# Kernel optimization log

Hardware: AMD Instinct MI355X
Metric: run time of the kernel (lower is better)

## Reference

```python
import jax, jax.numpy as jnp
import numpy as np

B, T_STEPS, H, W = 8192, 512, 64, 64


def setup_inputs() -> dict:
    key = jax.random.key(0)
    k_w, k_g, k_i, k_j, k_a = jax.random.split(key, 5)
    walls = (jax.random.uniform(k_w, (B, H, W)) < 0.3).astype(jnp.float32)
    walls = walls.at[:, 0, :].set(1.0).at[:, H - 1, :].set(1.0)
    walls = walls.at[:, :, 0].set(1.0).at[:, :, W - 1].set(1.0)
    # goals: sparse cells with value 10 (the code checks goals[...] == 10)
    goals = jnp.where(jax.random.uniform(k_g, (B, H, W)) < 0.02, 10.0, 0.0).astype(jnp.float32)
    # start positions strictly interior; clear the wall at each start cell
    i0 = jax.random.randint(k_i, (B,), 1, H - 1)
    j0 = jax.random.randint(k_j, (B,), 1, W - 1)
    walls = walls.at[jnp.arange(B), i0, j0].set(0.0)
    world = jnp.stack([walls, goals], axis=1)  # [B, 2, H, W]
    s0 = jnp.stack([i0, j0], axis=1).astype(jnp.float32)  # [B, 2]
    a = jax.random.randint(k_a, (B, T_STEPS), 0, 5).astype(jnp.int32)  # actions in {0..4}
    return {"s0": s0, "a": a, "world": world, "T": T_STEPS}


def _rollout(s0, a, world, T):
    walls = world[:, 0].reshape(world.shape[0], -1)  # [B, H*W]
    goals = world[:, 1].reshape(world.shape[0], -1)  # [B, H*W]
    Wd = world.shape[3]

    def step(s, a_t):
        # action deltas: 1 -> row-1, 2 -> row+1, 3 -> col-1, 4 -> col+1, 0 -> stay
        dr = jnp.where(a_t == 1, -1.0, jnp.where(a_t == 2, 1.0, 0.0))
        dc = jnp.where(a_t == 3, -1.0, jnp.where(a_t == 4, 1.0, 0.0))
        s_new = s + jnp.stack([dr, dc], axis=1).astype(s.dtype)  # [B, 2]
        idx = (s_new[:, 0].astype(jnp.int32) * Wd + s_new[:, 1].astype(jnp.int32))[:, None]
        g = jnp.take_along_axis(goals, idx, axis=1)[:, 0]
        w = jnp.take_along_axis(walls, idx, axis=1)[:, 0]
        hit_goal = g == 10.0
        hit_wall = jnp.logical_and(jnp.logical_not(hit_goal), w == 1.0)
        r = jnp.where(hit_goal, 1.0, jnp.where(hit_wall, -1.0, -0.01)).astype(jnp.float32)
        s_next = jnp.where(hit_wall[:, None], s, s_new)  # revert move on wall hit
        return s_next, (s_next, r)

    _, (s_traj, r_traj) = jax.lax.scan(step, s0, jnp.swapaxes(a[:, :T], 0, 1))
    s_full = jnp.concatenate([s0[:, None, :], jnp.swapaxes(s_traj, 0, 1)], axis=1)  # [B, T+1, 2]
    r0 = jnp.zeros((s0.shape[0], 1), dtype=jnp.float32)
    r_full = jnp.concatenate([r0, jnp.swapaxes(r_traj, 0, 1)], axis=1)  # [B, T+1]
    return s_full, r_full


def reference(s0, a, world, T):
    return _rollout(s0, a, world, T)
```

## Files before the change

kernel.cpp:

```cpp
#include <hip/hip_runtime.h>
#include <stdint.h>

#define T_STEPS 512
#define CELLS   4096
#define EPB     32
#define WPE     256
#define WPAD    257
#define ASTRIDE 130
#define SSTRIDE 66
#define RSTRIDE 33
#define CHUNK   32
#define NCHUNK  (T_STEPS / CHUNK)
#define KPC     (CHUNK / 4)

__device__ __forceinline__ uint32_t code4(float4 w, float4 g) {
    uint32_t b0 = (g.x == 10.0f) ? 2u : ((w.x == 1.0f) ? 1u : 0u);
    uint32_t b1 = (g.y == 10.0f) ? 2u : ((w.y == 1.0f) ? 1u : 0u);
    uint32_t b2 = (g.z == 10.0f) ? 2u : ((w.z == 1.0f) ? 1u : 0u);
    uint32_t b3 = (g.w == 10.0f) ? 2u : ((w.w == 1.0f) ? 1u : 0u);
    return b0 | (b1 << 2) | (b2 << 4) | (b3 << 6);
}

__global__ __launch_bounds__(64) void pack_kernel(
    const float* __restrict__ world, uint32_t* __restrict__ packed)
{
    const int b = blockIdx.x;
    const int t = threadIdx.x;
    const float* wbase = world + (size_t)b * (2 * CELLS);
    const float* gbase = wbase + CELLS;
    #pragma unroll
    for (int h = 0; h < 4; ++h) {
        const int w  = h * 64 + t;
        const int c0 = w * 16;
        uint32_t word = 0;
        #pragma unroll
        for (int j = 0; j < 4; ++j) {
            float4 wf = *(const float4*)(wbase + c0 + 4 * j);
            float4 gf = *(const float4*)(gbase + c0 + 4 * j);
            word |= code4(wf, gf) << (8 * j);
        }
        packed[(size_t)b * WPE + w] = word;
    }
}

__global__ __launch_bounds__(64) void rollout_kernel(
    const float* __restrict__ s0,
    const int*   __restrict__ act,
    const uint32_t* __restrict__ packed,
    float* __restrict__ out,
    int B)
{
    __shared__ uint32_t wlds[EPB * WPAD];
    __shared__ uint32_t alds[EPB * ASTRIDE];
    __shared__ float    sbuf[EPB * SSTRIDE];
    __shared__ float    rbuf[EPB * RSTRIDE];

    const int tid = threadIdx.x;
    const int b0  = blockIdx.x * EPB;

    for (int ee = 0; ee < EPB; ++ee) {
        uint4 v = *(const uint4*)(packed + (size_t)(b0 + ee) * WPE + tid * 4);
        const int base = ee * WPAD + tid * 4;
        wlds[base]     = v.x;
        wlds[base + 1] = v.y;
        wlds[base + 2] = v.z;
        wlds[base + 3] = v.w;
    }
    for (int ee = 0; ee < EPB; ++ee) {
        const int4* ap = (const int4*)(act + (size_t)(b0 + ee) * T_STEPS);
        const int4 x = ap[2 * tid];
        const int4 y = ap[2 * tid + 1];
        const uint32_t w0 = (uint32_t)(x.x & 255) | ((uint32_t)(x.y & 255) << 8)
                          | ((uint32_t)(x.z & 255) << 16) | ((uint32_t)(x.w & 255) << 24);
        const uint32_t w1 = (uint32_t)(y.x & 255) | ((uint32_t)(y.y & 255) << 8)
                          | ((uint32_t)(y.z & 255) << 16) | ((uint32_t)(y.w & 255) << 24);
        const int base = ee * ASTRIDE + 2 * tid;
        alds[base]     = w0;
        alds[base + 1] = w1;
    }
    __syncthreads();

    const int e = tid & (EPB - 1);
    const int b = b0 + e;
    float2 s = *(const float2*)(s0 + 2 * (size_t)b);
    int r = (int)s.x;
    int c = (int)s.y;
    int p = r * 64 + c;
    const uint32_t* my    = wlds + e * WPAD;
    const uint32_t* myact = alds + e * ASTRIDE;

    auto lookup = [&](int q) -> int {
        const int idx = q + ((q < 0) ? CELLS : 0);
        const uint32_t wd = my[(idx >> 4) & (WPE - 1)];
        const int cell = (wd >> ((idx & 15) * 2)) & 3;
        return ((unsigned)idx < (unsigned)CELLS) ? cell : 0;
    };

    float* const s_base = out;
    float* const r_base = out + (size_t)B * (2 * (T_STEPS + 1));

    if (tid < EPB) {
        *(float2*)(s_base + (size_t)b * (2 * (T_STEPS + 1))) = s;
        r_base[(size_t)b * (T_STEPS + 1)] = 0.0f;
    }

    uint32_t aw = myact[0];
    for (int chunk = 0; chunk < NCHUNK; ++chunk) {
        for (int k = 0; k < KPC; ++k) {
            const int kk = chunk * KPC + k;
            const uint32_t aw_next = myact[kk + 1];
            const int a0 = aw & 255, a1 = (aw >> 8) & 255;
            const int a2 = (aw >> 16) & 255, a3 = (aw >> 24) & 255;
            const int as4[4] = {a0, a1, a2, a3};
            #pragma unroll
            for (int jj = 0; jj < 2; ++jj) {
                const int ls = k * 4 + jj * 2;
                const int u0 = as4[2 * jj];
                const int u1 = as4[2 * jj + 1];
                const int d0r = (u0 == 1) ? -1 : ((u0 == 2) ? 1 : 0);
                const int d0c = (u0 == 3) ? -1 : ((u0 == 4) ? 1 : 0);
                const int d1r = (u1 == 1) ? -1 : ((u1 == 2) ? 1 : 0);
                const int d1c = (u1 == 3) ? -1 : ((u1 == 4) ? 1 : 0);
                const int e0 = d0r * 64 + d0c;
                const int e1 = d1r * 64 + d1c;
                const int q0  = p + e0;
                const int q10 = p + e1;
                const int q11 = q0 + e1;
                const int l0  = lookup(q0);
                const int l10 = lookup(q10);
                const int l11 = lookup(q11);
                const bool hw0  = (l0 == 1);
                const float rew0 = (l0 == 2) ? 1.0f : (hw0 ? -1.0f : -0.01f);
                const int p0  = hw0 ? p : q0;
                const int r0v = hw0 ? r : r + d0r;
                const int c0v = hw0 ? c : c + d0c;
                const int l1 = hw0 ? l10 : l11;
                const bool hw1  = (l1 == 1);
                const float rew1 = (l1 == 2) ? 1.0f : (hw1 ? -1.0f : -0.01f);
                p = hw1 ? p0 : p0 + e1;
                r = hw1 ? r0v : r0v + d1r;
                c = hw1 ? c0v : c0v + d1c;
                *(float2*)(&sbuf[e * SSTRIDE + 2 * ls]) =
                    make_float2((float)r0v, (float)c0v);
                *(float2*)(&sbuf[e * SSTRIDE + 2 * ls + 2]) =
                    make_float2((float)r, (float)c);
                rbuf[e * RSTRIDE + ls]     = rew0;
                rbuf[e * RSTRIDE + ls + 1] = rew1;
            }
            aw = aw_next;
        }
        __syncthreads();
        for (int ee = 0; ee < EPB; ++ee) {
            const float v = sbuf[ee * SSTRIDE + tid];
            s_base[(size_t)(b0 + ee) * (2 * (T_STEPS + 1)) + chunk * 64 + 2 + tid] = v;
        }
        for (int ee = 0; ee < EPB; ee += 2) {
            const int e2 = ee + (tid >> 5);
            const int j  = tid & 31;
            const float v = rbuf[e2 * RSTRIDE + j];
            r_base[(size_t)(b0 + e2) * (T_STEPS + 1) + chunk * 32 + 1 + j] = v;
        }
        __syncthreads();
    }
}

extern "C" void kernel_launch(void* const* d_in, const int* in_sizes, int n_in,
                              void* d_out, int out_size, void* d_ws, size_t ws_size,
                              hipStream_t stream) {
    const float* s0    = (const float*)d_in[0];
    const int*   act   = (const int*)d_in[1];
    const float* world = (const float*)d_in[2];
    float*       out   = (float*)d_out;
    uint32_t*    packed = (uint32_t*)d_ws;

    const int B = in_sizes[0] / 2;

    pack_kernel<<<B, 64, 0, stream>>>(world, packed);
    rollout_kernel<<<B / EPB, 64, 0, stream>>>(s0, act, packed, out, B);
}
```

Measured before the change: 443.8 us.

## Interleave two environments per lane and use a zero sentinel word for out-of-range lookups

Previously lanes 32-63 duplicated the work of lanes 0-31. Now each of the 16 lane groups steps two environments at once, interleaving their independent LDS lookups to raise ILP across the serial dependency chain. Out-of-range indices now read a padded sentinel word set to zero, replacing the per-lookup clamp-and-select. Each lane does twice as many serial steps, and lanes 16-63 all repeat the same work, so overall throughput depends on latency hiding.

New measurement: 475.6 us. +7.2%, slower.

```diff
diff --git a/kernel.cpp b/kernel.cpp
--- a/kernel.cpp
+++ b/kernel.cpp
@@ -66,6 +66,7 @@
         wlds[base + 2] = v.z;
         wlds[base + 3] = v.w;
     }
+    if (tid < EPB) wlds[tid * WPAD + WPE] = 0u;
     for (int ee = 0; ee < EPB; ++ee) {
         const int4* ap = (const int4*)(act + (size_t)(b0 + ee) * T_STEPS);
         const int4 x = ap[2 * tid];
@@ -80,74 +81,112 @@
     }
     __syncthreads();
 
-    const int e = tid & (EPB - 1);
-    const int b = b0 + e;
-    float2 s = *(const float2*)(s0 + 2 * (size_t)b);
-    int r = (int)s.x;
-    int c = (int)s.y;
-    int p = r * 64 + c;
-    const uint32_t* my    = wlds + e * WPAD;
-    const uint32_t* myact = alds + e * ASTRIDE;
-
-    auto lookup = [&](int q) -> int {
-        const int idx = q + ((q < 0) ? CELLS : 0);
-        const uint32_t wd = my[(idx >> 4) & (WPE - 1)];
-        const int cell = (wd >> ((idx & 15) * 2)) & 3;
-        return ((unsigned)idx < (unsigned)CELLS) ? cell : 0;
-    };
-
     float* const s_base = out;
     float* const r_base = out + (size_t)B * (2 * (T_STEPS + 1));
 
     if (tid < EPB) {
-        *(float2*)(s_base + (size_t)b * (2 * (T_STEPS + 1))) = s;
-        r_base[(size_t)b * (T_STEPS + 1)] = 0.0f;
-    }
-
-    uint32_t aw = myact[0];
+        const float2 si = *(const float2*)(s0 + 2 * (size_t)(b0 + tid));
+        *(float2*)(s_base + (size_t)(b0 + tid) * (2 * (T_STEPS + 1))) = si;
+        r_base[(size_t)(b0 + tid) * (T_STEPS + 1)] = 0.0f;
+    }
+
+    const int eA = 2 * (tid & 15);
+    const int eB = eA + 1;
+    const float2 sA = *(const float2*)(s0 + 2 * (size_t)(b0 + eA));
+    const float2 sB = *(const float2*)(s0 + 2 * (size_t)(b0 + eB));
+    int rA = (int)sA.x, cA = (int)sA.y, pA = rA * 64 + cA;
+    int rB = (int)sB.x, cB = (int)sB.y, pB = rB * 64 + cB;
+    const uint32_t* myA = wlds + eA * WPAD;
+    const uint32_t* myB = wlds + eB * WPAD;
+    const uint32_t* actA = alds + eA * ASTRIDE;
+    const uint32_t* actB = alds + eB * ASTRIDE;
+
+    auto waddr = [](int q) -> int {
+        const int w = (int)((((unsigned)q) >> 4) & 255u);
+        return ((unsigned)(q + CELLS) < 2u * CELLS) ? w : WPE;
+    };
+
+    uint32_t awA = actA[0];
+    uint32_t awB = actB[0];
     for (int chunk = 0; chunk < NCHUNK; ++chunk) {
         for (int k = 0; k < KPC; ++k) {
             const int kk = chunk * KPC + k;
-            const uint32_t aw_next = myact[kk + 1];
-            const int a0 = aw & 255, a1 = (aw >> 8) & 255;
-            const int a2 = (aw >> 16) & 255, a3 = (aw >> 24) & 255;
-            const int as4[4] = {a0, a1, a2, a3};
+            const uint32_t awA_n = actA[kk + 1];
+            const uint32_t awB_n = actB[kk + 1];
+            const int aA[4] = {(int)(awA & 255), (int)((awA >> 8) & 255),
+                               (int)((awA >> 16) & 255), (int)((awA >> 24) & 255)};
+            const int aB[4] = {(int)(awB & 255), (int)((awB >> 8) & 255),
+                               (int)((awB >> 16) & 255), (int)((awB >> 24) & 255)};
             #pragma unroll
             for (int jj = 0; jj < 2; ++jj) {
                 const int ls = k * 4 + jj * 2;
-                const int u0 = as4[2 * jj];
-                const int u1 = as4[2 * jj + 1];
-                const int d0r = (u0 == 1) ? -1 : ((u0 == 2) ? 1 : 0);
-                const int d0c = (u0 == 3) ? -1 : ((u0 == 4) ? 1 : 0);
-                const int d1r = (u1 == 1) ? -1 : ((u1 == 2) ? 1 : 0);
-                const int d1c = (u1 == 3) ? -1 : ((u1 == 4) ? 1 : 0);
-                const int e0 = d0r * 64 + d0c;
-                const int e1 = d1r * 64 + d1c;
-                const int q0  = p + e0;
-                const int q10 = p + e1;
-                const int q11 = q0 + e1;
-                const int l0  = lookup(q0);
-                const int l10 = lookup(q10);
-                const int l11 = lookup(q11);
-                const bool hw0  = (l0 == 1);
-                const float rew0 = (l0 == 2) ? 1.0f : (hw0 ? -1.0f : -0.01f);
-                const int p0  = hw0 ? p : q0;
-                const int r0v = hw0 ? r : r + d0r;
-                const int c0v = hw0 ? c : c + d0c;
-                const int l1 = hw0 ? l10 : l11;
-                const bool hw1  = (l1 == 1);
-                const float rew1 = (l1 == 2) ? 1.0f : (hw1 ? -1.0f : -0.01f);
-                p = hw1 ? p0 : p0 + e1;
-                r = hw1 ? r0v : r0v + d1r;
-                c = hw1 ? c0v : c0v + d1c;
-                *(float2*)(&sbuf[e * SSTRIDE + 2 * ls]) =
-                    make_float2((float)r0v, (float)c0v);
-                *(float2*)(&sbuf[e * SSTRIDE + 2 * ls + 2]) =
-                    make_float2((float)r, (float)c);
-                rbuf[e * RSTRIDE + ls]     = rew0;
-                rbuf[e * RSTRIDE + ls + 1] = rew1;
+                const int uA0 = aA[2 * jj], uA1 = aA[2 * jj + 1];
+                const int uB0 = aB[2 * jj], uB1 = aB[2 * jj + 1];
+                const int dA0r = (uA0 == 1) ? -1 : ((uA0 == 2) ? 1 : 0);
+                const int dA0c = (uA0 == 3) ? -1 : ((uA0 == 4) ? 1 : 0);
+                const int dA1r = (uA1 == 1) ? -1 : ((uA1 == 2) ? 1 : 0);
+                const int dA1c = (uA1 == 3) ? -1 : ((uA1 == 4) ? 1 : 0);
+                const int dB0r = (uB0 == 1) ? -1 : ((uB0 == 2) ? 1 : 0);
+                const int dB0c = (uB0 == 3) ? -1 : ((uB0 == 4) ? 1 : 0);
+                const int dB1r = (uB1 == 1) ? -1 : ((uB1 == 2) ? 1 : 0);
+                const int dB1c = (uB1 == 3) ? -1 : ((uB1 == 4) ? 1 : 0);
+                const int eAd0 = dA0r * 64 + dA0c, eAd1 = dA1r * 64 + dA1c;
+                const int eBd0 = dB0r * 64 + dB0c, eBd1 = dB1r * 64 + dB1c;
+                const int qA0 = pA + eAd0, qA10 = pA + eAd1, qA11 = qA0 + eAd1;
+                const uint32_t wA0  = myA[waddr(qA0)];
+                const uint32_t wA10 = myA[waddr(qA10)];
+                const uint32_t wA11 = myA[waddr(qA11)];
+                const int qB0 = pB + eBd0, qB10 = pB + eBd1, qB11 = qB0 + eBd1;
+                const uint32_t wB0  = myB[waddr(qB0)];
+                const uint32_t wB10 = myB[waddr(qB10)];
+                const uint32_t wB11 = myB[waddr(qB11)];
+                {
+                    const int l0 = (int)((wA0 >> ((qA0 & 15) * 2)) & 3);
+                    const bool hw0 = (l0 == 1);
+                    const float rew0 = (l0 == 2) ? 1.0f : (hw0 ? -1.0f : -0.01f);
+                    const int p0  = hw0 ? pA : qA0;
+                    const int r0v = hw0 ? rA : rA + dA0r;
+                    const int c0v = hw0 ? cA : cA + dA0c;
+                    const uint32_t W1 = hw0 ? wA10 : wA11;
+                    const int q1 = p0 + eAd1;
+                    const int l1 = (int)((W1 >> ((q1 & 15) * 2)) & 3);
+                    const bool hw1 = (l1 == 1);
+                    const float rew1 = (l1 == 2) ? 1.0f : (hw1 ? -1.0f : -0.01f);
+                    pA = hw1 ? p0 : q1;
+                    rA = hw1 ? r0v : r0v + dA1r;
+                    cA = hw1 ? c0v : c0v + dA1c;
+                    *(float2*)(&sbuf[eA * SSTRIDE + 2 * ls]) =
+                        make_float2((float)r0v, (float)c0v);
+                    *(float2*)(&sbuf[eA * SSTRIDE + 2 * ls + 2]) =
+                        make_float2((float)rA, (float)cA);
+                    rbuf[eA * RSTRIDE + ls]     = rew0;
+                    rbuf[eA * RSTRIDE + ls + 1] = rew1;
+                }
+                {
+                    const int l0 = (int)((wB0 >> ((qB0 & 15) * 2)) & 3);
+                    const bool hw0 = (l0 == 1);
+                    const float rew0 = (l0 == 2) ? 1.0f : (hw0 ? -1.0f : -0.01f);
+                    const int p0  = hw0 ? pB : qB0;
+                    const int r0v = hw0 ? rB : rB + dB0r;
+                    const int c0v = hw0 ? cB : cB + dB0c;
+                    const uint32_t W1 = hw0 ? wB10 : wB11;
+                    const int q1 = p0 + eBd1;
+                    const int l1 = (int)((W1 >> ((q1 & 15) * 2)) & 3);
+                    const bool hw1 = (l1 == 1);
+                    const float rew1 = (l1 == 2) ? 1.0f : (hw1 ? -1.0f : -0.01f);
+                    pB = hw1 ? p0 : q1;
+                    rB = hw1 ? r0v : r0v + dB1r;
+                    cB = hw1 ? c0v : c0v + dB1c;
+                    *(float2*)(&sbuf[eB * SSTRIDE + 2 * ls]) =
+                        make_float2((float)r0v, (float)c0v);
+                    *(float2*)(&sbuf[eB * SSTRIDE + 2 * ls + 2]) =
+                        make_float2((float)rB, (float)cB);
+                    rbuf[eB * RSTRIDE + ls]     = rew0;
+                    rbuf[eB * RSTRIDE + ls + 1] = rew1;
+                }
             }
-            aw = aw_next;
+            awA = awA_n;
+            awB = awB_n;
         }
         __syncthreads();
         for (int ee = 0; ee < EPB; ++ee) {
```
